# Optimization experiments

Hardware: AMD Instinct MI355X
Metric: run time of the kernel (lower is better)

Reference implementation:

```python
import jax, jax.numpy as jnp
import numpy as np

B, T, C, H = 2, 2048, 1024, 16
HD = C // H          # head dim = 64
HD2 = HD // 2        # rotary half = 32


def setup_inputs() -> dict:
    key = jax.random.key(0)
    k0, k1, k2 = jax.random.split(key, 3)
    x = jax.random.normal(k0, (B, T, C), jnp.float32)
    Wqkv = jax.random.normal(k1, (C, 3 * C), jnp.float32) * (1.0 / np.sqrt(C))
    bqkv = jnp.zeros((3 * C,), jnp.float32)
    Wproj = jax.random.normal(k2, (C, C), jnp.float32) * (1.0 / np.sqrt(C))
    bproj = jnp.zeros((C,), jnp.float32)
    # standard rotary frequencies: theta_i = 10000^{-2i/hd}
    inv_freq = 1.0 / (10000.0 ** (jnp.arange(0, HD, 2, dtype=jnp.float32) / HD))
    angles = jnp.arange(T, dtype=jnp.float32)[:, None] * inv_freq[None, :]  # (T, HD2)
    return {
        "x": x,
        "freqs_cos": jnp.cos(angles),
        "freqs_sin": jnp.sin(angles),
        "Wqkv": Wqkv,
        "bqkv": bqkv,
        "Wproj": Wproj,
        "bproj": bproj,
    }


def _rope(u, cos, sin):
    # u: (B, T, H, HD); half-split pairing: (u[i], u[i + HD/2]) form a complex pair
    u1, u2 = u[..., :HD2], u[..., HD2:]
    c = cos[None, :, None, :]  # (1, T, 1, HD2)
    s = sin[None, :, None, :]
    return jnp.concatenate([u1 * c - u2 * s, u1 * s + u2 * c], axis=-1)


def reference(x, freqs_cos, freqs_sin, Wqkv, bqkv, Wproj, bproj):
    Bc, Tc, Cc = x.shape
    qkv = x @ Wqkv + bqkv                      # (B, T, 3C)
    q, k, v = jnp.split(qkv, 3, axis=-1)
    q = q.reshape(Bc, Tc, H, HD)
    k = k.reshape(Bc, Tc, H, HD)
    v = v.reshape(Bc, Tc, H, HD)
    q = _rope(q, freqs_cos, freqs_sin)
    k = _rope(k, freqs_cos, freqs_sin)
    scale = 1.0 / np.sqrt(HD)
    scores = jnp.einsum("bthd,bshd->bhts", q, k) * scale  # (B, H, T, T)
    causal = jnp.tril(jnp.ones((Tc, Tc), dtype=bool))
    scores = jnp.where(causal[None, None], scores, jnp.finfo(scores.dtype).min)
    p = jax.nn.softmax(scores, axis=-1)
    y = jnp.einsum("bhts,bshd->bthd", p, v).reshape(Bc, Tc, Cc)
    return y @ Wproj + bproj
```

## Files before the change

### kernel.cpp

```cpp
#include <hip/hip_runtime.h>
#include <hip/hip_bf16.h>
#include <cstdint>
#include <cmath>

typedef __bf16 bf16_t;
typedef __attribute__((ext_vector_type(8))) __bf16 bf16x8;
typedef __attribute__((ext_vector_type(4))) float f32x4;

#define LOG2E 1.4426950408889634f

constexpr int B_ = 2, T_ = 2048, C_ = 1024, H_ = 16, HD_ = 64, HD2_ = 32;
constexpr int M_ = B_ * T_;

static __device__ __forceinline__ f32x4 mfma16(bf16x8 a, bf16x8 b, f32x4 c) {
    return __builtin_amdgcn_mfma_f32_16x16x32_bf16(a, b, c, 0, 0, 0);
}

#define GLL(gp, lp)                                                          \
    __builtin_amdgcn_global_load_lds(                                        \
        (const __attribute__((address_space(1))) void*)(gp),                 \
        (__attribute__((address_space(3))) void*)(lp), 16, 0, 0)

__global__ void cast_f32_to_bf16(const float* __restrict__ in, bf16_t* __restrict__ out, int n4) {
    int i = blockIdx.x * blockDim.x + threadIdx.x;
    if (i < n4) {
        float4 v = ((const float4*)in)[i];
        bf16_t o[4] = {(bf16_t)v.x, (bf16_t)v.y, (bf16_t)v.z, (bf16_t)v.w};
        *(uint64_t*)(out + (size_t)i * 4) = *(uint64_t*)o;
    }
}

__global__ void transpose_cast(const float* __restrict__ W, bf16_t* __restrict__ WT, int K, int N) {
    __shared__ float tile[32][33];
    int nb = blockIdx.x * 32, kb = blockIdx.y * 32;
    for (int i = threadIdx.y; i < 32; i += 8)
        tile[i][threadIdx.x] = W[(size_t)(kb + i) * N + nb + threadIdx.x];
    __syncthreads();
    for (int i = threadIdx.y; i < 32; i += 8)
        WT[(size_t)(nb + i) * K + kb + threadIdx.x] = (bf16_t)tile[threadIdx.x][i];
}

template <int MODE>
__global__ __launch_bounds__(256, 2) void gemm128(
    const bf16_t* __restrict__ A, const bf16_t* __restrict__ BT, const float* __restrict__ bias,
    int N, int K,
    bf16_t* __restrict__ Qb, bf16_t* __restrict__ Kb, bf16_t* __restrict__ VTb,
    const float* __restrict__ cosT, const float* __restrict__ sinT, float* __restrict__ out) {
    __shared__ alignas(16) bf16_t As[128 * 32];
    __shared__ alignas(16) bf16_t Bs[128 * 32];
    const int tid = threadIdx.x;
    const int w = tid >> 6, lane = tid & 63;
    const int quad = lane >> 4, r = lane & 15;
    const int wm = (w >> 1) * 64, wn = (w & 1) * 64;
    const int mb = blockIdx.y * 128, nb = blockIdx.x * 128;
    const int row_st = tid >> 2, seg = tid & 3;

    f32x4 acc[4][4] = {};

    const bf16_t* gA0 = A + (size_t)(mb + row_st) * K + seg * 8;
    const bf16_t* gA1 = A + (size_t)(mb + row_st + 64) * K + seg * 8;
    const bf16_t* gB0 = BT + (size_t)(nb + row_st) * K + seg * 8;
    const bf16_t* gB1 = BT + (size_t)(nb + row_st + 64) * K + seg * 8;

    for (int k0 = 0; k0 < K; k0 += 32) {
        __syncthreads();
        GLL(gA0 + k0, As + tid * 8);
        GLL(gA1 + k0, As + 2048 + tid * 8);
        GLL(gB0 + k0, Bs + tid * 8);
        GLL(gB1 + k0, Bs + 2048 + tid * 8);
        __syncthreads();
        bf16x8 af[4], bfr[4];
#pragma unroll
        for (int i = 0; i < 4; i++) af[i] = *(const bf16x8*)(As + (wm + i * 16 + r) * 32 + quad * 8);
#pragma unroll
        for (int j = 0; j < 4; j++) bfr[j] = *(const bf16x8*)(Bs + (wn + j * 16 + r) * 32 + quad * 8);
#pragma unroll
        for (int i = 0; i < 4; i++)
#pragma unroll
            for (int j = 0; j < 4; j++) acc[i][j] = mfma16(af[i], bfr[j], acc[i][j]);
    }

    if (MODE == 0) {
        const int col_base = nb + wn;
        const int region = col_base >> 10;
        const int h = (col_base & 1023) >> 6;
        const float qscale = 0.125f * LOG2E;
        if (region < 2) {
#pragma unroll
            for (int i = 0; i < 4; i++) {
#pragma unroll
                for (int g = 0; g < 4; g++) {
                    int m = mb + wm + i * 16 + quad * 4 + g;
                    int b = m >> 11, t = m & (T_ - 1);
                    bf16_t* dst = (region == 0 ? Qb : Kb) + ((size_t)((b * H_ + h) * T_ + t)) * 64;
                    int tw = t & 7;
#pragma unroll
                    for (int j = 0; j < 2; j++) {
                        int d = j * 16 + r;
                        float u1 = acc[i][j][g] + bias[col_base + d];
                        float u2 = acc[i][j + 2][g] + bias[col_base + d + 32];
                        float c = cosT[t * HD2_ + d], s = sinT[t * HD2_ + d];
                        float o1 = u1 * c - u2 * s;
                        float o2 = u1 * s + u2 * c;
                        if (region == 0) {
                            dst[d] = (bf16_t)(o1 * qscale);
                            dst[d + 32] = (bf16_t)(o2 * qscale);
                        } else {
                            dst[((((d >> 3) ^ tw)) << 3) | (d & 7)] = (bf16_t)o1;
                            dst[(((((d + 32) >> 3) ^ tw)) << 3) | (d & 7)] = (bf16_t)o2;
                        }
                    }
                }
            }
        } else {
#pragma unroll
            for (int i = 0; i < 4; i++) {
                int m0 = mb + wm + i * 16 + quad * 4;
                int b = m0 >> 11, t0 = m0 & (T_ - 1);
                bf16_t* base = VTb + (size_t)(b * H_ + h) * 64 * T_;
#pragma unroll
                for (int j = 0; j < 4; j++) {
                    int d = j * 16 + r;
                    float bb = bias[col_base + d];
                    bf16_t pk[4];
#pragma unroll
                    for (int g = 0; g < 4; g++) pk[g] = (bf16_t)(acc[i][j][g] + bb);
                    int c = (((t0 >> 3) & 7) ^ (d & 7));
                    int tsw = (t0 & ~63) | (c << 3) | (t0 & 7);
                    *(uint64_t*)(base + (size_t)d * T_ + tsw) = *(uint64_t*)pk;
                }
            }
        }
    } else {
#pragma unroll
        for (int i = 0; i < 4; i++)
#pragma unroll
            for (int g = 0; g < 4; g++) {
                int m = mb + wm + i * 16 + quad * 4 + g;
#pragma unroll
                for (int j = 0; j < 4; j++) {
                    int col = nb + wn + j * 16 + r;
                    out[(size_t)m * N + col] = acc[i][j][g] + bias[col];
                }
            }
    }
}

__global__ __launch_bounds__(256, 2) void attn64(
    const bf16_t* __restrict__ Qb, const bf16_t* __restrict__ Kb,
    const bf16_t* __restrict__ VTb, bf16_t* __restrict__ att) {
    __shared__ alignas(16) bf16_t Ks[2][64 * 64];
    __shared__ alignas(16) bf16_t Vs[2][64 * 64];
    __shared__ alignas(16) bf16_t Ps[4][1024];
    const int tid = threadIdx.x;
    const int w = tid >> 6, lane = tid & 63;
    const int quad = lane >> 4, r = lane & 15;
    const int pt = blockIdx.x;
    const int bh = blockIdx.y;
    const size_t kbase = (size_t)bh * T_ * 64;
    const size_t vbase = (size_t)bh * 64 * T_;
    bf16_t* Pw = &Ps[w][0];
    const int srow = tid >> 3, schunk = tid & 7;
    const int koff0 = ((quad ^ (r & 7)) * 8);
    const int koff1 = (((quad + 4) ^ (r & 7)) * 8);

    for (int half = 0; half < 2; half++) {
        const int qt = half ? (31 - pt) : pt;
        const int q0 = qt * 64;
        const int qrow = q0 + w * 16 + r;
        bf16x8 qf0 = *(const bf16x8*)(Qb + kbase + (size_t)qrow * 64 + quad * 8);
        bf16x8 qf1 = *(const bf16x8*)(Qb + kbase + (size_t)qrow * 64 + 32 + quad * 8);
        f32x4 oacc[4] = {};
        float mstate = -INFINITY, lstate = 0.f;
        const int n = qt + 1;

        __syncthreads();
        {
            const bf16_t* kg = Kb + kbase + (size_t)srow * 64 + schunk * 8;
            GLL(kg, &Ks[0][0] + tid * 8);
            GLL(kg + 32 * 64, &Ks[0][0] + 2048 + tid * 8);
            const bf16_t* vg = VTb + vbase + (size_t)srow * T_ + schunk * 8;
            GLL(vg, &Vs[0][0] + tid * 8);
            GLL(vg + (size_t)32 * T_, &Vs[0][0] + 2048 + tid * 8);
        }
        for (int jt = 0; jt < n; jt++) {
            const int cur = jt & 1;
            const int j0 = jt * 64;
            __syncthreads();
            if (jt + 1 < n) {
                const int j0n = j0 + 64;
                const bf16_t* kg = Kb + kbase + (size_t)(j0n + srow) * 64 + schunk * 8;
                GLL(kg, &Ks[cur ^ 1][0] + tid * 8);
                GLL(kg + 32 * 64, &Ks[cur ^ 1][0] + 2048 + tid * 8);
                const bf16_t* vg = VTb + vbase + (size_t)srow * T_ + j0n + schunk * 8;
                GLL(vg, &Vs[cur ^ 1][0] + tid * 8);
                GLL(vg + (size_t)32 * T_, &Vs[cur ^ 1][0] + 2048 + tid * 8);
            }
            f32x4 s[4];
#pragma unroll
            for (int m0 = 0; m0 < 4; m0++) {
                const bf16_t* kp = &Ks[cur][(m0 * 16 + r) * 64];
                bf16x8 kf0 = *(const bf16x8*)(kp + koff0);
                bf16x8 kf1 = *(const bf16x8*)(kp + koff1);
                f32x4 z = {0.f, 0.f, 0.f, 0.f};
                z = mfma16(kf0, qf0, z);
                z = mfma16(kf1, qf1, z);
                s[m0] = z;
            }
            if (jt == qt) {
#pragma unroll
                for (int m0 = 0; m0 < 4; m0++) {
                    int kvb = j0 + m0 * 16 + quad * 4;
#pragma unroll
                    for (int g = 0; g < 4; g++)
                        if (kvb + g > qrow) s[m0][g] = -INFINITY;
                }
            }
            float vm = -INFINITY;
#pragma unroll
            for (int m0 = 0; m0 < 4; m0++)
#pragma unroll
                for (int g = 0; g < 4; g++) vm = fmaxf(vm, s[m0][g]);
            vm = fmaxf(vm, __shfl_xor(vm, 16));
            vm = fmaxf(vm, __shfl_xor(vm, 32));
            float mnew = fmaxf(mstate, vm);
            float alpha = __builtin_amdgcn_exp2f(mstate - mnew);
            float rs = 0.f;
#pragma unroll
            for (int m0 = 0; m0 < 4; m0++)
#pragma unroll
                for (int g = 0; g < 4; g++) {
                    float p = __builtin_amdgcn_exp2f(s[m0][g] - mnew);
                    s[m0][g] = p;
                    rs += p;
                }
            rs += __shfl_xor(rs, 16);
            rs += __shfl_xor(rs, 32);
            lstate = lstate * alpha + rs;
            mstate = mnew;
#pragma unroll
            for (int d0 = 0; d0 < 4; d0++)
#pragma unroll
                for (int g = 0; g < 4; g++) oacc[d0][g] *= alpha;
#pragma unroll
            for (int m0 = 0; m0 < 4; m0++) {
                bf16_t hq[4];
#pragma unroll
                for (int g = 0; g < 4; g++) hq[g] = (bf16_t)s[m0][g];
                int elem = (m0 >> 1) * 512 + (((m0 & 1) * 2 + (quad >> 1)) * 16 + r) * 8 + (quad & 1) * 4;
                *(uint64_t*)(Pw + elem) = *(uint64_t*)hq;
            }
            __builtin_amdgcn_wave_barrier();
            bf16x8 pf0 = *(const bf16x8*)(Pw + lane * 8);
            bf16x8 pf1 = *(const bf16x8*)(Pw + 512 + lane * 8);
#pragma unroll
            for (int d0 = 0; d0 < 4; d0++) {
                const bf16_t* vp = &Vs[cur][(d0 * 16 + r) * 64];
                bf16x8 vf0 = *(const bf16x8*)(vp + koff0);
                bf16x8 vf1 = *(const bf16x8*)(vp + koff1);
                oacc[d0] = mfma16(vf0, pf0, oacc[d0]);
                oacc[d0] = mfma16(vf1, pf1, oacc[d0]);
            }
            __builtin_amdgcn_wave_barrier();
        }
        int b = bh >> 4, h = bh & 15;
        float inv = 1.f / lstate;
        bf16_t* dst = att + ((size_t)(b * T_ + qrow)) * 1024 + h * 64;
#pragma unroll
        for (int d0 = 0; d0 < 4; d0++) {
            bf16_t hh[4];
#pragma unroll
            for (int g = 0; g < 4; g++) hh[g] = (bf16_t)(oacc[d0][g] * inv);
            *(uint64_t*)(dst + d0 * 16 + quad * 4) = *(uint64_t*)hh;
        }
    }
}

extern "C" void kernel_launch(void* const* d_in, const int* in_sizes, int n_in,
                              void* d_out, int out_size, void* d_ws, size_t ws_size,
                              hipStream_t stream) {
    const float* x = (const float*)d_in[0];
    const float* fcos = (const float*)d_in[1];
    const float* fsin = (const float*)d_in[2];
    const float* Wqkv = (const float*)d_in[3];
    const float* bqkv = (const float*)d_in[4];
    const float* Wproj = (const float*)d_in[5];
    const float* bproj = (const float*)d_in[6];
    float* out = (float*)d_out;

    uint8_t* p = (uint8_t*)d_ws;
    size_t need = 0;
    auto take = [&](size_t bytes) {
        void* q = p;
        size_t pad = (bytes + 255) & ~(size_t)255;
        p += pad;
        need += pad;
        return q;
    };
    bf16_t* xb = (bf16_t*)take((size_t)M_ * C_ * 2);
    bf16_t* wqkvT = (bf16_t*)take((size_t)3 * C_ * C_ * 2);
    bf16_t* wprojT = (bf16_t*)take((size_t)C_ * C_ * 2);
    bf16_t* Qb = (bf16_t*)take((size_t)B_ * H_ * T_ * 64 * 2);
    bf16_t* Kb = (bf16_t*)take((size_t)B_ * H_ * T_ * 64 * 2);
    bf16_t* VTb = (bf16_t*)take((size_t)B_ * H_ * 64 * T_ * 2);
    bf16_t* attb = (bf16_t*)take((size_t)M_ * C_ * 2);
    if (ws_size < need) return;

    cast_f32_to_bf16<<<(M_ * C_ / 4 + 255) / 256, 256, 0, stream>>>(x, xb, M_ * C_ / 4);
    transpose_cast<<<dim3(3 * C_ / 32, C_ / 32), dim3(32, 8), 0, stream>>>(Wqkv, wqkvT, C_, 3 * C_);
    transpose_cast<<<dim3(C_ / 32, C_ / 32), dim3(32, 8), 0, stream>>>(Wproj, wprojT, C_, C_);

    gemm128<0><<<dim3(3 * C_ / 128, M_ / 128), 256, 0, stream>>>(
        xb, wqkvT, bqkv, 3 * C_, C_, Qb, Kb, VTb, fcos, fsin, nullptr);

    attn64<<<dim3(16, B_ * H_), 256, 0, stream>>>(Qb, Kb, VTb, attb);

    gemm128<1><<<dim3(C_ / 128, M_ / 128), 256, 0, stream>>>(
        attb, wprojT, bproj, C_, C_, nullptr, nullptr, nullptr, nullptr, nullptr, out);
}
```

Measured before the change: 204.7 us.

## Split attention KV across two wave groups, fuse prep kernels, raise gemm occupancy

```diff
diff --git a/kernel.cpp b/kernel.cpp
--- a/kernel.cpp
+++ b/kernel.cpp
@@ -21,27 +21,40 @@
         (const __attribute__((address_space(1))) void*)(gp),                 \
         (__attribute__((address_space(3))) void*)(lp), 16, 0, 0)
 
-__global__ void cast_f32_to_bf16(const float* __restrict__ in, bf16_t* __restrict__ out, int n4) {
-    int i = blockIdx.x * blockDim.x + threadIdx.x;
-    if (i < n4) {
-        float4 v = ((const float4*)in)[i];
+__global__ void prep(const float* __restrict__ x, bf16_t* __restrict__ xb,
+                     const float* __restrict__ Wqkv, bf16_t* __restrict__ wqkvT,
+                     const float* __restrict__ Wproj, bf16_t* __restrict__ wprojT) {
+    __shared__ float tile[32][33];
+    const int bid = blockIdx.x, tid = threadIdx.x;
+    if (bid < 4096) {
+        int i = bid * 256 + tid;
+        float4 v = ((const float4*)x)[i];
         bf16_t o[4] = {(bf16_t)v.x, (bf16_t)v.y, (bf16_t)v.z, (bf16_t)v.w};
-        *(uint64_t*)(out + (size_t)i * 4) = *(uint64_t*)o;
-    }
-}
-
-__global__ void transpose_cast(const float* __restrict__ W, bf16_t* __restrict__ WT, int K, int N) {
-    __shared__ float tile[32][33];
-    int nb = blockIdx.x * 32, kb = blockIdx.y * 32;
-    for (int i = threadIdx.y; i < 32; i += 8)
-        tile[i][threadIdx.x] = W[(size_t)(kb + i) * N + nb + threadIdx.x];
+        *(uint64_t*)(xb + (size_t)i * 4) = *(uint64_t*)o;
+        return;
+    }
+    const float* W;
+    bf16_t* WT;
+    int K, N, nb, kb;
+    if (bid < 4096 + 3072) {
+        int t = bid - 4096;
+        W = Wqkv; WT = wqkvT; K = C_; N = 3 * C_;
+        nb = (t % 96) * 32; kb = (t / 96) * 32;
+    } else {
+        int t = bid - 7168;
+        W = Wproj; WT = wprojT; K = C_; N = C_;
+        nb = (t & 31) * 32; kb = (t >> 5) * 32;
+    }
+    int tx = tid & 31, ty = tid >> 5;
+    for (int i = ty; i < 32; i += 8)
+        tile[i][tx] = W[(size_t)(kb + i) * N + nb + tx];
     __syncthreads();
-    for (int i = threadIdx.y; i < 32; i += 8)
-        WT[(size_t)(nb + i) * K + kb + threadIdx.x] = (bf16_t)tile[threadIdx.x][i];
+    for (int i = ty; i < 32; i += 8)
+        WT[(size_t)(nb + i) * K + kb + tx] = (bf16_t)tile[tx][i];
 }
 
 template <int MODE>
-__global__ __launch_bounds__(256, 2) void gemm128(
+__global__ __launch_bounds__(256, 3) void gemm128(
     const bf16_t* __restrict__ A, const bf16_t* __restrict__ BT, const float* __restrict__ bias,
     int N, int K,
     bf16_t* __restrict__ Qb, bf16_t* __restrict__ Kb, bf16_t* __restrict__ VTb,
@@ -146,17 +159,20 @@
     }
 }
 
-__global__ __launch_bounds__(256, 2) void attn64(
+__global__ __launch_bounds__(512, 4) void attn64(
     const bf16_t* __restrict__ Qb, const bf16_t* __restrict__ Kb,
     const bf16_t* __restrict__ VTb, bf16_t* __restrict__ att) {
-    __shared__ alignas(16) bf16_t Ks[2][64 * 64];
-    __shared__ alignas(16) bf16_t Vs[2][64 * 64];
-    __shared__ alignas(16) bf16_t Ps[4][1024];
+    __shared__ alignas(16) bf16_t Ks[2][2][4096];
+    __shared__ alignas(16) bf16_t Vs[2][2][4096];
+    __shared__ alignas(16) bf16_t Ps[8][1024];
     const int tid = threadIdx.x;
     const int w = tid >> 6, lane = tid & 63;
+    const int grp = w >> 2, wq = w & 3;
     const int quad = lane >> 4, r = lane & 15;
-    const int pt = blockIdx.x;
-    const int bh = blockIdx.y;
+    const int id = blockIdx.x;
+    const int t = 31 - (id >> 5);
+    const int bh = id & 31;
+    const int ntiles = t + 1, nstages = (t + 2) >> 1;
     const size_t kbase = (size_t)bh * T_ * 64;
     const size_t vbase = (size_t)bh * 64 * T_;
     bf16_t* Pw = &Ps[w][0];
@@ -164,80 +180,84 @@
     const int koff0 = ((quad ^ (r & 7)) * 8);
     const int koff1 = (((quad + 4) ^ (r & 7)) * 8);
 
-    for (int half = 0; half < 2; half++) {
-        const int qt = half ? (31 - pt) : pt;
-        const int q0 = qt * 64;
-        const int qrow = q0 + w * 16 + r;
-        bf16x8 qf0 = *(const bf16x8*)(Qb + kbase + (size_t)qrow * 64 + quad * 8);
-        bf16x8 qf1 = *(const bf16x8*)(Qb + kbase + (size_t)qrow * 64 + 32 + quad * 8);
-        f32x4 oacc[4] = {};
-        float mstate = -INFINITY, lstate = 0.f;
-        const int n = qt + 1;
-
+    const int qrow = t * 64 + wq * 16 + r;
+    bf16x8 qf0 = *(const bf16x8*)(Qb + kbase + (size_t)qrow * 64 + quad * 8);
+    bf16x8 qf1 = *(const bf16x8*)(Qb + kbase + (size_t)qrow * 64 + 32 + quad * 8);
+
+    f32x4 oacc[4] = {};
+    float m = -INFINITY, l = 0.f;
+
+    {
+        const bf16_t* kg = Kb + kbase + (size_t)srow * 64 + schunk * 8;
+        GLL(kg, &Ks[0][0][0] + tid * 8);
+        const bf16_t* vg = VTb + vbase + (size_t)srow * T_ + schunk * 8;
+        GLL(vg, &Vs[0][0][0] + tid * 8);
+        if (1 < ntiles) {
+            GLL(kg + 64 * 64, &Ks[0][1][0] + tid * 8);
+            GLL(vg + 64, &Vs[0][1][0] + tid * 8);
+        }
+    }
+    for (int s = 0; s < nstages; s++) {
+        const int cur = s & 1;
         __syncthreads();
-        {
-            const bf16_t* kg = Kb + kbase + (size_t)srow * 64 + schunk * 8;
-            GLL(kg, &Ks[0][0] + tid * 8);
-            GLL(kg + 32 * 64, &Ks[0][0] + 2048 + tid * 8);
-            const bf16_t* vg = VTb + vbase + (size_t)srow * T_ + schunk * 8;
-            GLL(vg, &Vs[0][0] + tid * 8);
-            GLL(vg + (size_t)32 * T_, &Vs[0][0] + 2048 + tid * 8);
-        }
-        for (int jt = 0; jt < n; jt++) {
-            const int cur = jt & 1;
-            const int j0 = jt * 64;
-            __syncthreads();
-            if (jt + 1 < n) {
-                const int j0n = j0 + 64;
-                const bf16_t* kg = Kb + kbase + (size_t)(j0n + srow) * 64 + schunk * 8;
-                GLL(kg, &Ks[cur ^ 1][0] + tid * 8);
-                GLL(kg + 32 * 64, &Ks[cur ^ 1][0] + 2048 + tid * 8);
-                const bf16_t* vg = VTb + vbase + (size_t)srow * T_ + j0n + schunk * 8;
-                GLL(vg, &Vs[cur ^ 1][0] + tid * 8);
-                GLL(vg + (size_t)32 * T_, &Vs[cur ^ 1][0] + 2048 + tid * 8);
-            }
-            f32x4 s[4];
+        if (s + 1 < nstages) {
+            const int ja = 2 * (s + 1);
+            const bf16_t* kg = Kb + kbase + (size_t)(ja * 64 + srow) * 64 + schunk * 8;
+            const bf16_t* vg = VTb + vbase + (size_t)srow * T_ + ja * 64 + schunk * 8;
+            GLL(kg, &Ks[cur ^ 1][0][0] + tid * 8);
+            GLL(vg, &Vs[cur ^ 1][0][0] + tid * 8);
+            if (ja + 1 < ntiles) {
+                GLL(kg + 64 * 64, &Ks[cur ^ 1][1][0] + tid * 8);
+                GLL(vg + 64, &Vs[cur ^ 1][1][0] + tid * 8);
+            }
+        }
+        const int jt = 2 * s + grp;
+        if (jt < ntiles) {
+            const bf16_t* Kt = &Ks[cur][grp][0];
+            const bf16_t* Vt = &Vs[cur][grp][0];
+            f32x4 sc[4];
 #pragma unroll
             for (int m0 = 0; m0 < 4; m0++) {
-                const bf16_t* kp = &Ks[cur][(m0 * 16 + r) * 64];
+                const bf16_t* kp = Kt + (m0 * 16 + r) * 64;
                 bf16x8 kf0 = *(const bf16x8*)(kp + koff0);
                 bf16x8 kf1 = *(const bf16x8*)(kp + koff1);
                 f32x4 z = {0.f, 0.f, 0.f, 0.f};
                 z = mfma16(kf0, qf0, z);
                 z = mfma16(kf1, qf1, z);
-                s[m0] = z;
-            }
-            if (jt == qt) {
+                sc[m0] = z;
+            }
+            if (jt == t) {
+                const int j0 = jt * 64;
 #pragma unroll
                 for (int m0 = 0; m0 < 4; m0++) {
                     int kvb = j0 + m0 * 16 + quad * 4;
 #pragma unroll
                     for (int g = 0; g < 4; g++)
-                        if (kvb + g > qrow) s[m0][g] = -INFINITY;
+                        if (kvb + g > qrow) sc[m0][g] = -INFINITY;
                 }
             }
             float vm = -INFINITY;
 #pragma unroll
             for (int m0 = 0; m0 < 4; m0++)
 #pragma unroll
-                for (int g = 0; g < 4; g++) vm = fmaxf(vm, s[m0][g]);
+                for (int g = 0; g < 4; g++) vm = fmaxf(vm, sc[m0][g]);
             vm = fmaxf(vm, __shfl_xor(vm, 16));
             vm = fmaxf(vm, __shfl_xor(vm, 32));
-            float mnew = fmaxf(mstate, vm);
-            float alpha = __builtin_amdgcn_exp2f(mstate - mnew);
+            float mnew = fmaxf(m, vm);
+            float alpha = __builtin_amdgcn_exp2f(m - mnew);
             float rs = 0.f;
 #pragma unroll
             for (int m0 = 0; m0 < 4; m0++)
 #pragma unroll
                 for (int g = 0; g < 4; g++) {
-                    float p = __builtin_amdgcn_exp2f(s[m0][g] - mnew);
-                    s[m0][g] = p;
-                    rs += p;
+                    float pp = __builtin_amdgcn_exp2f(sc[m0][g] - mnew);
+                    sc[m0][g] = pp;
+                    rs += pp;
                 }
             rs += __shfl_xor(rs, 16);
             rs += __shfl_xor(rs, 32);
-            lstate = lstate * alpha + rs;
-            mstate = mnew;
+            l = l * alpha + rs;
+            m = mnew;
 #pragma unroll
             for (int d0 = 0; d0 < 4; d0++)
 #pragma unroll
@@ -246,7 +266,7 @@
             for (int m0 = 0; m0 < 4; m0++) {
                 bf16_t hq[4];
 #pragma unroll
-                for (int g = 0; g < 4; g++) hq[g] = (bf16_t)s[m0][g];
+                for (int g = 0; g < 4; g++) hq[g] = (bf16_t)sc[m0][g];
                 int elem = (m0 >> 1) * 512 + (((m0 & 1) * 2 + (quad >> 1)) * 16 + r) * 8 + (quad & 1) * 4;
                 *(uint64_t*)(Pw + elem) = *(uint64_t*)hq;
             }
@@ -255,7 +275,7 @@
             bf16x8 pf1 = *(const bf16x8*)(Pw + 512 + lane * 8);
 #pragma unroll
             for (int d0 = 0; d0 < 4; d0++) {
-                const bf16_t* vp = &Vs[cur][(d0 * 16 + r) * 64];
+                const bf16_t* vp = Vt + (d0 * 16 + r) * 64;
                 bf16x8 vf0 = *(const bf16x8*)(vp + koff0);
                 bf16x8 vf1 = *(const bf16x8*)(vp + koff1);
                 oacc[d0] = mfma16(vf0, pf0, oacc[d0]);
@@ -263,14 +283,33 @@
             }
             __builtin_amdgcn_wave_barrier();
         }
-        int b = bh >> 4, h = bh & 15;
-        float inv = 1.f / lstate;
+    }
+    __syncthreads();
+    float* Co = (float*)&Ks[0][0][0];
+    float* Cm = (float*)&Vs[0][0][0];
+    float* Cl = Cm + 64;
+    if (grp == 1) {
+#pragma unroll
+        for (int d0 = 0; d0 < 4; d0++)
+            *(f32x4*)(Co + wq * 1024 + r * 64 + d0 * 16 + quad * 4) = oacc[d0];
+        if (quad == 0) { Cm[wq * 16 + r] = m; Cl[wq * 16 + r] = l; }
+    }
+    __syncthreads();
+    if (grp == 0) {
+        float m1 = Cm[wq * 16 + r], l1 = Cl[wq * 16 + r];
+        float mm = fmaxf(m, m1);
+        float a0 = __builtin_amdgcn_exp2f(m - mm);
+        float a1 = __builtin_amdgcn_exp2f(m1 - mm);
+        float inv = 1.f / (l * a0 + l1 * a1);
+        const int b = bh >> 4, h = bh & 15;
         bf16_t* dst = att + ((size_t)(b * T_ + qrow)) * 1024 + h * 64;
 #pragma unroll
         for (int d0 = 0; d0 < 4; d0++) {
+            f32x4 o1 = *(const f32x4*)(Co + wq * 1024 + r * 64 + d0 * 16 + quad * 4);
             bf16_t hh[4];
 #pragma unroll
-            for (int g = 0; g < 4; g++) hh[g] = (bf16_t)(oacc[d0][g] * inv);
+            for (int g = 0; g < 4; g++)
+                hh[g] = (bf16_t)((oacc[d0][g] * a0 + o1[g] * a1) * inv);
             *(uint64_t*)(dst + d0 * 16 + quad * 4) = *(uint64_t*)hh;
         }
     }
@@ -306,14 +345,12 @@
     bf16_t* attb = (bf16_t*)take((size_t)M_ * C_ * 2);
     if (ws_size < need) return;
 
-    cast_f32_to_bf16<<<(M_ * C_ / 4 + 255) / 256, 256, 0, stream>>>(x, xb, M_ * C_ / 4);
-    transpose_cast<<<dim3(3 * C_ / 32, C_ / 32), dim3(32, 8), 0, stream>>>(Wqkv, wqkvT, C_, 3 * C_);
-    transpose_cast<<<dim3(C_ / 32, C_ / 32), dim3(32, 8), 0, stream>>>(Wproj, wprojT, C_, C_);
+    prep<<<8192, 256, 0, stream>>>(x, xb, Wqkv, wqkvT, Wproj, wprojT);
 
     gemm128<0><<<dim3(3 * C_ / 128, M_ / 128), 256, 0, stream>>>(
         xb, wqkvT, bqkv, 3 * C_, C_, Qb, Kb, VTb, fcos, fsin, nullptr);
 
-    attn64<<<dim3(16, B_ * H_), 256, 0, stream>>>(Qb, Kb, VTb, attb);
+    attn64<<<dim3(1024), 512, 0, stream>>>(Qb, Kb, VTb, attb);
 
     gemm128<1><<<dim3(C_ / 128, M_ / 128), 256, 0, stream>>>(
         attb, wprojT, bproj, C_, C_, nullptr, nullptr, nullptr, nullptr, nullptr, out);
```

New measurement: 191.4 us. 1.07x faster.
